# Kernel optimization log

Measured on AMD Instinct MI355X. Metric: run time of the kernel, lower is better.

## Reference

```python
import jax, jax.numpy as jnp
import numpy as np

DN = ('NCH', 'OIH', 'NCH')

def conv1d(x, w, b, stride, pad):
    y = jax.lax.conv_general_dilated(x, w, (stride,), [(pad, pad)], dimension_numbers=DN)
    return y + b[None, :, None]

def deconv1d(x, w, b):
    # ConvTranspose1d(k=3, stride=2, padding=1, output_padding=1): L -> 2L
    # expressed as lhs-dilated conv with padding (k-1-p, k-1-p+output_padding) = (1, 2)
    y = jax.lax.conv_general_dilated(x, w, (1,), [(1, 2)], lhs_dilation=(2,), dimension_numbers=DN)
    return y + b[None, :, None]

def setup_inputs() -> dict:
    key = jax.random.key(0)
    ks = jax.random.split(key, 24)
    B, T, A = 256, 512, 32
    H = 256              # hidden_dim / embedding_dim
    K = 8192             # n_embeddings
    enc_ch = [64, 128, 256]
    dec_ch = [256, 128, 64]
    s = 0.05
    inp = {'x': jax.random.normal(ks[0], (B, T, A), jnp.float32)}
    # encoder convs (OIH layout), k=3
    in_ch = A
    for i, ch in enumerate(enc_ch):
        inp[f'enc_w{i}'] = jax.random.normal(ks[1 + 2 * i], (ch, in_ch, 3), jnp.float32) * s
        inp[f'enc_b{i}'] = jnp.zeros((ch,), jnp.float32)
        in_ch = ch
    inp['proj_w'] = jax.random.normal(ks[8], (H, enc_ch[-1], 1), jnp.float32) * s
    inp['proj_b'] = jnp.zeros((H,), jnp.float32)
    inp['embedding'] = jax.random.normal(ks[9], (K, H), jnp.float32)
    # decoder deconvs (stored directly in conv OIH form)
    in_ch = H
    for i, ch in enumerate(dec_ch + [A]):
        inp[f'dec_w{i}'] = jax.random.normal(ks[10 + 2 * i], (ch, in_ch, 3), jnp.float32) * s
        inp[f'dec_b{i}'] = jnp.zeros((ch,), jnp.float32)
        in_ch = ch
    return inp

def _forward(x, enc_w0, enc_b0, enc_w1, enc_b1, enc_w2, enc_b2, proj_w, proj_b,
             embedding, dec_w0, dec_b0, dec_w1, dec_b1, dec_w2, dec_b2, dec_w3, dec_b3):
    # ---- encoder ----
    h = jnp.transpose(x, (0, 2, 1))                      # (B, A, T)
    h = jax.nn.relu(conv1d(h, enc_w0, enc_b0, 2, 1))
    h = jax.nn.relu(conv1d(h, enc_w1, enc_b1, 2, 1))
    h = jax.nn.relu(conv1d(h, enc_w2, enc_b2, 2, 1))
    z_e = conv1d(h, proj_w, proj_b, 1, 0)                # (B, H, T/8)
    # ---- EMA vector quantizer (eval-mode math) ----
    B, C, T = z_e.shape
    flat = jnp.transpose(z_e, (0, 2, 1)).reshape(-1, C)  # (B*T, C)
    dist = (jnp.sum(flat * flat, axis=1, keepdims=True)
            - 2.0 * flat @ embedding.T
            + jnp.sum(embedding * embedding, axis=1))    # (B*T, K)
    indices = jnp.argmin(dist, axis=1)                   # (B*T,)
    z_q = embedding[indices].reshape(B, T, C).transpose(0, 2, 1)  # (B, C, T)
    commitment_loss = jnp.mean((jax.lax.stop_gradient(z_e) - z_q) ** 2)
    codebook_loss = jnp.mean((z_e - jax.lax.stop_gradient(z_q)) ** 2)
    z_q = z_e + jax.lax.stop_gradient(z_q - z_e)         # straight-through
    # ---- decoder ----
    d = jax.nn.relu(deconv1d(z_q, dec_w0, dec_b0))
    d = jax.nn.relu(deconv1d(d, dec_w1, dec_b1))
    d = jax.nn.relu(deconv1d(d, dec_w2, dec_b2))
    d = deconv1d(d, dec_w3, dec_b3)                      # (B, A, seq_len)
    out = jnp.transpose(d, (0, 2, 1))                    # (B, seq_len, A)
    return out, codebook_loss, commitment_loss, indices.reshape(B, T)

def reference(x, enc_w0, enc_b0, enc_w1, enc_b1, enc_w2, enc_b2, proj_w, proj_b,
              embedding, dec_w0, dec_b0, dec_w1, dec_b1, dec_w2, dec_b2, dec_w3, dec_b3):
    return _forward(x, enc_w0, enc_b0, enc_w1, enc_b1, enc_w2, enc_b2, proj_w, proj_b,
                    embedding, dec_w0, dec_b0, dec_w1, dec_b1, dec_w2, dec_b2, dec_w3, dec_b3)
```

## Files before the change

kernel.cpp:

```cpp
#include <hip/hip_runtime.h>


typedef _Float16 half8 __attribute__((ext_vector_type(8)));
typedef _Float16 half4v __attribute__((ext_vector_type(4)));
typedef float f32x4 __attribute__((ext_vector_type(4)));
typedef float f32x16 __attribute__((ext_vector_type(16)));

struct CP2 {
  const _Float16* inH; const _Float16* inL;
  const _Float16* wH; const _Float16* wL;
  const float* bias;
  float* outF; _Float16* outH; _Float16* outL;
  const int* vidx;
  int Ci, lg2Ci, Ti, Co, To, K2, stride, pad, lg2U, Umask;
};

template<int SP, int PAR, bool GATHER, bool RELU, int OM>
__global__ __launch_bounds__(256, 4) void conv_mfma(CP2 p) {
  __shared__ _Float16 As[SP * 64 * 40];
  __shared__ _Float16 Bs[SP * 64 * 40];
  const int tid = threadIdx.x;
  const int wv = tid >> 6;
  const int lane = tid & 63;
  const int m = lane & 15, q = lane >> 4;
  const int btbase = blockIdx.x * 64;
  const int cobase = blockIdx.y * 64;
  f32x4 acc[4];
#pragma unroll
  for (int j = 0; j < 4; ++j) acc[j] = {0.f, 0.f, 0.f, 0.f};

  const int nkb = p.K2 >> 5;
  for (int kb = 0; kb < nkb; ++kb) {
    const int k0 = kb << 5;
    const int tap = k0 >> p.lg2Ci;
    const int ci0 = k0 & (p.Ci - 1);
    int dt;
    if (PAR == 0)      { dt = 0; }
    else if (PAR == 1) { dt = tap; }
    else               { dt = tap - p.pad; }
    __syncthreads();
    {
      const int wb = (blockIdx.y * nkb + kb) * 2048 + tid * 8;
      *(uint4*)&Bs[(tid >> 2) * 40 + (tid & 3) * 8] = *(const uint4*)&p.wH[wb];
      if (SP == 2)
        *(uint4*)&Bs[64 * 40 + (tid >> 2) * 40 + (tid & 3) * 8] = *(const uint4*)&p.wL[wb];
    }
    {
      const int r = tid >> 2, g = tid & 3;
      const int bt = btbase + r;
      const int b = bt >> p.lg2U, u = bt & p.Umask;
      const int tin = (PAR < 0) ? u * p.stride + dt : u + dt;
      const bool ok = (tin >= 0) && (tin < p.Ti);
      int ai;
      if (GATHER) {
        const int er = ok ? p.vidx[b * p.Ti + tin] : 0;
        ai = er * 256 + ci0 + g * 8;
      } else {
        ai = (b * p.Ti + tin) * p.Ci + ci0 + g * 8;
      }
      const uint4 z = {0u, 0u, 0u, 0u};
      const uint4 vh = ok ? *(const uint4*)&p.inH[ai] : z;
      *(uint4*)&As[r * 40 + g * 8] = vh;
      if (SP == 2) {
        const uint4 vl = ok ? *(const uint4*)&p.inL[ai] : z;
        *(uint4*)&As[64 * 40 + r * 40 + g * 8] = vl;
      }
    }
    __syncthreads();
    const int row = wv * 16 + m;
    const half8 a1 = *(const half8*)&As[row * 40 + q * 8];
    half8 a2;
    if (SP == 2) a2 = *(const half8*)&As[64 * 40 + row * 40 + q * 8];
#pragma unroll
    for (int ct = 0; ct < 4; ++ct) {
      const half8 b1 = *(const half8*)&Bs[(ct * 16 + m) * 40 + q * 8];
      half8 b2;
      if (SP == 2) b2 = *(const half8*)&Bs[64 * 40 + (ct * 16 + m) * 40 + q * 8];
      acc[ct] = __builtin_amdgcn_mfma_f32_16x16x32_f16(a1, b1, acc[ct], 0, 0, 0);
      if (SP == 2) {
        acc[ct] = __builtin_amdgcn_mfma_f32_16x16x32_f16(a2, b1, acc[ct], 0, 0, 0);
        acc[ct] = __builtin_amdgcn_mfma_f32_16x16x32_f16(a1, b2, acc[ct], 0, 0, 0);
      }
    }
  }
#pragma unroll
  for (int ct = 0; ct < 4; ++ct) {
    const int co = cobase + ct * 16 + m;
    if (co < p.Co) {
      const float bv = p.bias[co];
#pragma unroll
      for (int j = 0; j < 4; ++j) {
        const int row = btbase + wv * 16 + q * 4 + j;
        const int b = row >> p.lg2U, u = row & p.Umask;
        float v = acc[ct][j] + bv;
        if (RELU) v = fmaxf(v, 0.f);
        const int t = (PAR < 0) ? u : 2 * u + PAR;
        const int oi = (b * p.To + t) * p.Co + co;
        if (OM == 3) {
          p.outF[oi] = v;
        } else if (OM == 1) {
          p.outH[oi] = (_Float16)v;
        } else {
          const _Float16 h = (_Float16)v;
          const _Float16 l = (_Float16)(v - (float)h);
          p.outH[oi] = h; p.outL[oi] = l;
        }
      }
    }
  }
}

struct CPD {
  const _Float16* inH; const _Float16* wS; const float* bias;
  float* outF; _Float16* outH;
  int Ci, Ti, Co, To, lg2U, Umask;
};

template<bool RELU, bool F32OUT>
__global__ __launch_bounds__(256, 4) void conv_dec(CPD p) {
  __shared__ _Float16 As[65 * 40];
  __shared__ _Float16 Bs[3 * 64 * 40];
  const int tid = threadIdx.x;
  const int wv = tid >> 6;
  const int lane = tid & 63;
  const int m = lane & 15, q = lane >> 4;
  const int btbase = blockIdx.x * 64;
  const int cobase = blockIdx.y * 64;
  const int b0 = btbase >> p.lg2U;
  const int u0 = btbase & p.Umask;
  f32x4 aE[4], aO[4];
#pragma unroll
  for (int j = 0; j < 4; ++j) { aE[j] = {0.f,0.f,0.f,0.f}; aO[j] = {0.f,0.f,0.f,0.f}; }

  const int nkb = p.Ci >> 5;
  for (int kb = 0; kb < nkb; ++kb) {
    const int ci0 = kb << 5;
    __syncthreads();
    {
      const int wb = (blockIdx.y * nkb + kb) * 6144 + tid * 8;
      const int ld = (tid >> 2) * 40 + (tid & 3) * 8;
#pragma unroll
      for (int tap = 0; tap < 3; ++tap)
        *(uint4*)&Bs[tap * 2560 + ld] = *(const uint4*)&p.wS[wb + tap * 2048];
    }
#pragma unroll
    for (int i = 0; i < 2; ++i) {
      const int e = i * 256 + tid;
      const int r = e >> 2, g = e & 3;
      if (r < 65) {
        const int ur = u0 + r;
        const bool ok = ur < p.Ti;
        const uint4 z = {0u, 0u, 0u, 0u};
        const uint4 v = ok ? *(const uint4*)&p.inH[(b0 * p.Ti + ur) * p.Ci + ci0 + g * 8] : z;
        *(uint4*)&As[r * 40 + g * 8] = v;
      }
    }
    __syncthreads();
    const int row = wv * 16 + m;
    const half8 a0  = *(const half8*)&As[row * 40 + q * 8];
    const half8 a1s = *(const half8*)&As[(row + 1) * 40 + q * 8];
#pragma unroll
    for (int ct = 0; ct < 4; ++ct) {
      const int c = ct * 16 + m;
      const half8 w0 = *(const half8*)&Bs[c * 40 + q * 8];
      const half8 w1 = *(const half8*)&Bs[2560 + c * 40 + q * 8];
      const half8 w2 = *(const half8*)&Bs[5120 + c * 40 + q * 8];
      aE[ct] = __builtin_amdgcn_mfma_f32_16x16x32_f16(a0,  w1, aE[ct], 0, 0, 0);
      aO[ct] = __builtin_amdgcn_mfma_f32_16x16x32_f16(a0,  w0, aO[ct], 0, 0, 0);
      aO[ct] = __builtin_amdgcn_mfma_f32_16x16x32_f16(a1s, w2, aO[ct], 0, 0, 0);
    }
  }
#pragma unroll
  for (int ct = 0; ct < 4; ++ct) {
    const int co = cobase + ct * 16 + m;
    if (co < p.Co) {
      const float bv = p.bias[co];
#pragma unroll
      for (int j = 0; j < 4; ++j) {
        const int u = u0 + wv * 16 + q * 4 + j;
        float vE = aE[ct][j] + bv;
        float vO = aO[ct][j] + bv;
        if (RELU) { vE = fmaxf(vE, 0.f); vO = fmaxf(vO, 0.f); }
        const int oiE = (b0 * p.To + 2 * u) * p.Co + co;
        const int oiO = oiE + p.Co;
        if (F32OUT) { p.outF[oiE] = vE; p.outF[oiO] = vO; }
        else        { p.outH[oiE] = (_Float16)vE; p.outH[oiO] = (_Float16)vO; }
      }
    }
  }
}


__global__ __launch_bounds__(256) void x_prep(const float* __restrict__ x,
                                              _Float16* __restrict__ h,
                                              _Float16* __restrict__ l) {
  const int i = blockIdx.x * 256 + threadIdx.x;
  const float4 v = ((const float4*)x)[i];
  half4v a, b;
  a.x = (_Float16)v.x; b.x = (_Float16)(v.x - (float)a.x);
  a.y = (_Float16)v.y; b.y = (_Float16)(v.y - (float)a.y);
  a.z = (_Float16)v.z; b.z = (_Float16)(v.z - (float)a.z);
  a.w = (_Float16)v.w; b.w = (_Float16)(v.w - (float)a.w);
  ((half4v*)h)[i] = a;
  ((half4v*)l)[i] = b;
}

struct WPE { const float* w; int dh, dl, Ci, lg2Ci, KWO, Co, PAR, SP, nkb, base, dec; };
struct WPA { WPE e[9]; };

__global__ __launch_bounds__(256) void w_prep(WPA a, _Float16* __restrict__ wst) {
  const int b = (int)blockIdx.x;
  int i = 0;
#pragma unroll
  for (int j = 1; j < 9; ++j) if (b >= a.e[j].base) i = j;
  const WPE E = a.e[i];
  const int local = b - E.base;
  const int cb = local / E.nkb;
  const int kb = local - cb * E.nkb;
  const int tid = threadIdx.x;
  const int cc = tid >> 2, g = tid & 3;
  const int co = cb * 64 + cc;
  const bool okc = co < E.Co;
  const int k0 = kb << 5;
  const int tap0 = k0 >> E.lg2Ci;
  const int ci0 = k0 & (E.Ci - 1);
  if (!E.dec) {
    const int ko = (E.PAR == 0) ? 1 : (E.PAR == 1 ? 2 * tap0 : tap0);
    half8 hv, lv;
#pragma unroll
    for (int j = 0; j < 8; ++j) {
      const float wv = okc ? E.w[(co * E.Ci + ci0 + g * 8 + j) * E.KWO + ko] : 0.f;
      hv[j] = (_Float16)wv;
      lv[j] = (_Float16)(wv - (float)hv[j]);
    }
    const int off = (cb * E.nkb + kb) * 2048 + tid * 8;
    *(half8*)&wst[E.dh + off] = hv;
    if (E.SP == 2) *(half8*)&wst[E.dl + off] = lv;
  } else {
#pragma unroll
    for (int tap = 0; tap < 3; ++tap) {
      half8 hv;
#pragma unroll
      for (int j = 0; j < 8; ++j) {
        const float wv = okc ? E.w[(co * E.Ci + ci0 + g * 8 + j) * 3 + tap] : 0.f;
        hv[j] = (_Float16)wv;
      }
      *(half8*)&wst[E.dh + ((cb * E.nkb + kb) * 3 + tap) * 2048 + tid * 8] = hv;
    }
  }
}

__global__ __launch_bounds__(256) void emb_prep(const float* __restrict__ emb,
                                                _Float16* __restrict__ hi,
                                                _Float16* __restrict__ lo,
                                                float* __restrict__ nrm) {
  const int k = blockIdx.x * 4 + (threadIdx.x >> 6);
  const int lane = threadIdx.x & 63;
  const int i = k * 64 + lane;
  const float4 v = ((const float4*)emb)[i];
  half4v a, b;
  a.x = (_Float16)v.x; b.x = (_Float16)(v.x - (float)a.x);
  a.y = (_Float16)v.y; b.y = (_Float16)(v.y - (float)a.y);
  a.z = (_Float16)v.z; b.z = (_Float16)(v.z - (float)a.z);
  a.w = (_Float16)v.w; b.w = (_Float16)(v.w - (float)a.w);
  ((half4v*)hi)[i] = a;
  ((half4v*)lo)[i] = b;
  double s = (double)v.x * v.x + (double)v.y * v.y +
             (double)v.z * v.z + (double)v.w * v.w;
  for (int off = 32; off; off >>= 1) s += __shfl_down(s, off);
  if (lane == 0) nrm[k] = (float)s;
}

__global__ __launch_bounds__(256, 2) void vq_mfma(const _Float16* __restrict__ z1g,
                                                  const _Float16* __restrict__ z2g,
                                                  const _Float16* __restrict__ e1g,
                                                  const _Float16* __restrict__ e2g,
                                                  const float* __restrict__ nrm,
                                                  float* __restrict__ pbest,
                                                  int* __restrict__ pidx) {
  __shared__ _Float16 es[2 * 2 * 4096];
  const int tid = threadIdx.x;
  const int lane = tid & 63;
  const int w = tid >> 6;
  const int m32 = lane & 31;
  const int hi = lane >> 5;
  const int seg = blockIdx.x & 7, rb = blockIdx.x >> 3;
  const int rbase = rb * 128;
  const int row_g = rbase + w * 32 + m32;

  half8 za[16], zb[16];
#pragma unroll
  for (int c = 0; c < 16; ++c) {
    const int zi = row_g * 256 + c * 16 + hi * 8;
    za[c] = *(const half8*)&z1g[zi];
    zb[c] = *(const half8*)&z2g[zi];
  }

  float best[16]; int bk[16];
#pragma unroll
  for (int i = 0; i < 16; ++i) { best[i] = 3.4e38f; bk[i] = 0; }

  const int sbase = (seg * 1024 + ((tid >> 7) & 1) * 32 + (tid & 31)) * 256
                  + ((tid >> 6) & 1) * 16 + ((tid >> 5) & 1) * 8;
  const int lw = w * 512;

  auto stage = [&](int cc_, int kb_, int buf_) {
    const int off = sbase + cc_ * 32768 + kb_ * 32;
    __builtin_amdgcn_global_load_lds(
        (const __attribute__((address_space(1))) void*)(e1g + off),
        (__attribute__((address_space(3))) void*)&es[(buf_ * 2 + 0) * 4096 + lw], 16, 0, 0);
    __builtin_amdgcn_global_load_lds(
        (const __attribute__((address_space(1))) void*)(e1g + off + 16384),
        (__attribute__((address_space(3))) void*)&es[(buf_ * 2 + 0) * 4096 + 2048 + lw], 16, 0, 0);
    __builtin_amdgcn_global_load_lds(
        (const __attribute__((address_space(1))) void*)(e2g + off),
        (__attribute__((address_space(3))) void*)&es[(buf_ * 2 + 1) * 4096 + lw], 16, 0, 0);
    __builtin_amdgcn_global_load_lds(
        (const __attribute__((address_space(1))) void*)(e2g + off + 16384),
        (__attribute__((address_space(3))) void*)&es[(buf_ * 2 + 1) * 4096 + 2048 + lw], 16, 0, 0);
  };

  stage(0, 0, 0);

  const int lb = lane * 8;
  f32x16 acc[4];
  for (int cc = 0; cc < 8; ++cc) {
    const int cbase = seg * 1024 + cc * 128;
#pragma unroll
    for (int ct = 0; ct < 4; ++ct) {
#pragma unroll
      for (int rg = 0; rg < 16; ++rg) acc[ct][rg] = 0.f;
    }
#pragma unroll
    for (int kb = 0; kb < 8; ++kb) {
      const int buf = kb & 1;
      const _Float16* e1s = &es[(buf * 2 + 0) * 4096];
      const _Float16* e2s = &es[(buf * 2 + 1) * 4096];
      __syncthreads();
      if (kb < 7)      stage(cc, kb + 1, buf ^ 1);
      else if (cc < 7) stage(cc + 1, 0, buf ^ 1);
      __builtin_amdgcn_s_setprio(1);
#pragma unroll
      for (int ct = 0; ct < 4; ++ct) {
#pragma unroll
        for (int k16 = 0; k16 < 2; ++k16) {
          const half8 b1 = *(const half8*)&e1s[ct * 1024 + k16 * 512 + lb];
          const half8 b2 = *(const half8*)&e2s[ct * 1024 + k16 * 512 + lb];
          const half8 a1 = za[kb * 2 + k16];
          const half8 a2 = zb[kb * 2 + k16];
          acc[ct] = __builtin_amdgcn_mfma_f32_32x32x16_f16(a1, b1, acc[ct], 0, 0, 0);
          acc[ct] = __builtin_amdgcn_mfma_f32_32x32x16_f16(a2, b1, acc[ct], 0, 0, 0);
          acc[ct] = __builtin_amdgcn_mfma_f32_32x32x16_f16(a1, b2, acc[ct], 0, 0, 0);
        }
      }
      __builtin_amdgcn_s_setprio(0);
    }
#pragma unroll
    for (int ct = 0; ct < 4; ++ct) {
      const int k = cbase + ct * 32 + m32;
      const float nv = nrm[k];
#pragma unroll
      for (int rg = 0; rg < 16; ++rg) {
        const float d = nv - 2.f * acc[ct][rg];
        if (d < best[rg]) { best[rg] = d; bk[rg] = k; }
      }
    }
  }
#pragma unroll
  for (int rg = 0; rg < 16; ++rg) {
    float bv = best[rg]; int kv = bk[rg];
    for (int off = 1; off < 32; off <<= 1) {
      const float ob = __shfl_xor(bv, off);
      const int ok = __shfl_xor(kv, off);
      if (ob < bv || (ob == bv && ok < kv)) { bv = ob; kv = ok; }
    }
    if (m32 == 0) {
      const int row = rbase + w * 32 + (rg & 3) + 8 * (rg >> 2) + 4 * hi;
      pbest[seg * 16384 + row] = bv;
      pidx[seg * 16384 + row] = kv;
    }
  }
}

__global__ void merge_kernel(const float* __restrict__ pbest, const int* __restrict__ pidx,
                             int* __restrict__ vidx, float* __restrict__ out_idx,
                             float* __restrict__ lacc) {
  const int n = blockIdx.x * 256 + threadIdx.x;
  float bv = pbest[n]; int kv = pidx[n];
#pragma unroll
  for (int s = 1; s < 8; ++s) {
    const float ob = pbest[s * 16384 + n];
    const int ok = pidx[s * 16384 + n];
    if (ob < bv || (ob == bv && ok < kv)) { bv = ob; kv = ok; }
  }
  vidx[n] = kv;
  out_idx[n] = (float)kv;
  if (n == 0) *lacc = 0.f;
}

__global__ __launch_bounds__(256) void loss_kernel(const _Float16* __restrict__ z1g,
                                                   const _Float16* __restrict__ z2g,
                                                   const float* __restrict__ emb,
                                                   const int* __restrict__ vidx,
                                                   float* __restrict__ lacc) {
  const int g4 = blockIdx.x * 256 + threadIdx.x;
  const int e0 = g4 * 4;
  const int n = e0 >> 8, c = e0 & 255;
  const half4v a = ((const half4v*)z1g)[g4];
  const half4v b = ((const half4v*)z2g)[g4];
  const float4 q4 = *(const float4*)&emb[vidx[n] * 256 + c];
  const float dx = ((float)a.x + (float)b.x) - q4.x;
  const float dy = ((float)a.y + (float)b.y) - q4.y;
  const float dz = ((float)a.z + (float)b.z) - q4.z;
  const float dw = ((float)a.w + (float)b.w) - q4.w;
  float s = dx * dx + dy * dy + dz * dz + dw * dw;
  for (int off = 32; off; off >>= 1) s += __shfl_down(s, off);
  __shared__ float red[4];
  if ((threadIdx.x & 63) == 0) red[threadIdx.x >> 6] = s;
  __syncthreads();
  if (threadIdx.x == 0) atomicAdd(lacc, red[0] + red[1] + red[2] + red[3]);
}

__global__ void fin_kernel(const float* __restrict__ lacc, float* __restrict__ out, int loff) {
  if (threadIdx.x == 0) {
    const float l = *lacc * (1.f / 4194304.f);
    out[loff] = l;
    out[loff + 1] = l;
  }
}

extern "C" void kernel_launch(void* const* d_in, const int* in_sizes, int n_in,
                              void* d_out, int out_size, void* d_ws, size_t ws_size,
                              hipStream_t stream) {
  const float* x   = (const float*)d_in[0];
  const float* ew0 = (const float*)d_in[1];  const float* eb0 = (const float*)d_in[2];
  const float* ew1 = (const float*)d_in[3];  const float* eb1 = (const float*)d_in[4];
  const float* ew2 = (const float*)d_in[5];  const float* eb2 = (const float*)d_in[6];
  const float* pw  = (const float*)d_in[7];  const float* pb  = (const float*)d_in[8];
  const float* emb = (const float*)d_in[9];
  const float* dw0 = (const float*)d_in[10]; const float* db0 = (const float*)d_in[11];
  const float* dw1 = (const float*)d_in[12]; const float* db1 = (const float*)d_in[13];
  const float* dw2 = (const float*)d_in[14]; const float* db2 = (const float*)d_in[15];
  const float* dw3 = (const float*)d_in[16]; const float* db3 = (const float*)d_in[17];
  float* ws  = (float*)d_ws;
  float* out = (float*)d_out;

  const int A0 = 0, B0 = 4194304, C0 = 8388608, TL = 12582912;
  _Float16* h0h = (_Float16*)(ws + C0);
  _Float16* h0l = h0h + 4194304;
  _Float16* h1h = (_Float16*)(ws + B0);
  _Float16* h1l = h1h + 4194304;
  _Float16* h2h = (_Float16*)(ws + A0);
  _Float16* h2l = h2h + 4194304;
  _Float16* h3h = (_Float16*)(ws + B0);
  _Float16* h3l = h3h + 4194304;
  _Float16* z1g = (_Float16*)(ws + A0);
  _Float16* z2g = z1g + 4194304;
  _Float16* e1g = (_Float16*)(ws + B0);
  _Float16* e2g = e1g + 2097152;
  float* pbest = ws + B0 + 2097152;
  int*   pidx  = (int*)(ws + B0 + 2097152 + 131072);
  _Float16* d1h = (_Float16*)(ws + C0);
  _Float16* d2h = (_Float16*)(ws + A0);
  _Float16* d3h = (_Float16*)(ws + B0);
  float* nrm  = ws + TL;
  int*   vidx = (int*)(ws + TL + 8192);
  float* lacc = ws + TL + 8192 + 16384;
  _Float16* wst = (_Float16*)(ws + TL + 32768);

  const int W_E0H = 0,      W_E0L = 6144;
  const int W_E1H = 12288,  W_E1L = 36864;
  const int W_E2H = 61440,  W_E2L = 159744;
  const int W_PJH = 258048, W_PJL = 323584;
  const int W_D0A = 389120, W_D0B = 454656;
  const int W_DC1 = 585728, W_DC2 = 684032, W_DC3 = 708608;

  const int idx_off  = out_size - 16384;
  const int loss_off = out_size - 16386;

  x_prep<<<4096, 256, 0, stream>>>(x, h0h, h0l);
  WPA wa;
  wa.e[0] = {ew0, W_E0H, W_E0L, 32,  5, 3, 64,  -1, 2, 3,  0,   0};
  wa.e[1] = {ew1, W_E1H, W_E1L, 64,  6, 3, 128, -1, 2, 6,  3,   0};
  wa.e[2] = {ew2, W_E2H, W_E2L, 128, 7, 3, 256, -1, 2, 12, 15,  0};
  wa.e[3] = {pw,  W_PJH, W_PJL, 256, 8, 1, 256, -1, 2, 8,  63,  0};
  wa.e[4] = {dw0, W_D0A, 0,     256, 8, 3, 256,  0, 1, 8,  95,  0};
  wa.e[5] = {dw0, W_D0B, 0,     256, 8, 3, 256,  1, 1, 16, 127, 0};
  wa.e[6] = {dw1, W_DC1, 0,     256, 8, 3, 128, -1, 1, 8,  191, 1};
  wa.e[7] = {dw2, W_DC2, 0,     128, 7, 3, 64,  -1, 1, 4,  207, 1};
  wa.e[8] = {dw3, W_DC3, 0,     64,  6, 3, 32,  -1, 1, 2,  211, 1};
  w_prep<<<213, 256, 0, stream>>>(wa, wst);

  CP2 p; p.vidx = nullptr; p.inH = nullptr; p.inL = nullptr;
  p.outF = nullptr; p.outH = nullptr; p.outL = nullptr;

  p.inH = h0h; p.inL = h0l; p.wH = wst + W_E0H; p.wL = wst + W_E0L;
  p.bias = eb0; p.outH = h1h; p.outL = h1l;
  p.Ci = 32; p.lg2Ci = 5; p.Ti = 512; p.Co = 64; p.To = 256;
  p.K2 = 96; p.stride = 2; p.pad = 1; p.lg2U = 8; p.Umask = 255;
  conv_mfma<2, -1, false, true, 0><<<dim3(1024, 1), 256, 0, stream>>>(p);

  p.inH = h1h; p.inL = h1l; p.wH = wst + W_E1H; p.wL = wst + W_E1L;
  p.bias = eb1; p.outH = h2h; p.outL = h2l;
  p.Ci = 64; p.lg2Ci = 6; p.Ti = 256; p.Co = 128; p.To = 128; p.K2 = 192;
  p.lg2U = 7; p.Umask = 127;
  conv_mfma<2, -1, false, true, 0><<<dim3(512, 2), 256, 0, stream>>>(p);

  p.inH = h2h; p.inL = h2l; p.wH = wst + W_E2H; p.wL = wst + W_E2L;
  p.bias = eb2; p.outH = h3h; p.outL = h3l;
  p.Ci = 128; p.lg2Ci = 7; p.Ti = 128; p.Co = 256; p.To = 64; p.K2 = 384;
  p.lg2U = 6; p.Umask = 63;
  conv_mfma<2, -1, false, true, 0><<<dim3(256, 4), 256, 0, stream>>>(p);

  p.inH = h3h; p.inL = h3l; p.wH = wst + W_PJH; p.wL = wst + W_PJL;
  p.bias = pb; p.outH = z1g; p.outL = z2g;
  p.Ci = 256; p.lg2Ci = 8; p.Ti = 64; p.Co = 256; p.To = 64;
  p.K2 = 256; p.stride = 1; p.pad = 0; p.lg2U = 6; p.Umask = 63;
  conv_mfma<2, -1, false, false, 0><<<dim3(256, 4), 256, 0, stream>>>(p);

  emb_prep<<<2048, 256, 0, stream>>>(emb, e1g, e2g, nrm);
  vq_mfma<<<1024, 256, 0, stream>>>(z1g, z2g, e1g, e2g, nrm, pbest, pidx);
  merge_kernel<<<64, 256, 0, stream>>>(pbest, pidx, vidx, out + idx_off, lacc);
  loss_kernel<<<4096, 256, 0, stream>>>(z1g, z2g, emb, vidx, lacc);
  fin_kernel<<<1, 64, 0, stream>>>(lacc, out, loss_off);

  p.inH = e1g; p.inL = nullptr; p.bias = db0;
  p.outH = d1h; p.outL = nullptr; p.vidx = vidx;
  p.Ci = 256; p.lg2Ci = 8; p.Ti = 64; p.Co = 256; p.To = 128;
  p.lg2U = 6; p.Umask = 63;
  p.wH = wst + W_D0A; p.wL = nullptr;
  p.K2 = 256; conv_mfma<1, 0, true, true, 1><<<dim3(256, 4), 256, 0, stream>>>(p);
  p.wH = wst + W_D0B;
  p.K2 = 512; conv_mfma<1, 1, true, true, 1><<<dim3(256, 4), 256, 0, stream>>>(p);

  CPD d;
  d.inH = d1h; d.wS = wst + W_DC1; d.bias = db1; d.outF = nullptr; d.outH = d2h;
  d.Ci = 256; d.Ti = 128; d.Co = 128; d.To = 256; d.lg2U = 7; d.Umask = 127;
  conv_dec<true, false><<<dim3(512, 2), 256, 0, stream>>>(d);

  d.inH = d2h; d.wS = wst + W_DC2; d.bias = db2; d.outH = d3h;
  d.Ci = 128; d.Ti = 256; d.Co = 64; d.To = 512; d.lg2U = 8; d.Umask = 255;
  conv_dec<true, false><<<dim3(1024, 1), 256, 0, stream>>>(d);

  d.inH = d3h; d.wS = wst + W_DC3; d.bias = db3; d.outF = out; d.outH = nullptr;
  d.Ci = 64; d.Ti = 512; d.Co = 32; d.To = 1024; d.lg2U = 9; d.Umask = 511;
  conv_dec<false, true><<<dim3(2048, 1), 256, 0, stream>>>(d);
}
```

Baseline: 515.5 us.

## Double-buffer conv tiles using direct global-to-LDS loads

Both conv kernels now stage activation and weight tiles with direct global-to-LDS loads into two LDS buffers. The next K-block is prefetched while the current one feeds the MFMAs, leaving one barrier per iteration instead of two. Weights are pre-arranged into MFMA fragment order, and out-of-range rows read from a small zeroed pad buffer, so LDS reads become contiguous per lane. The aim is to hide global load latency and drop the register round-trip. The cost is twice the LDS per block, and correctness relies on the compiler inserting the right waits for the asynchronous LDS loads before each barrier.

```diff
diff --git a/kernel.cpp b/kernel.cpp
--- a/kernel.cpp
+++ b/kernel.cpp
@@ -6,10 +6,14 @@
 typedef float f32x4 __attribute__((ext_vector_type(4)));
 typedef float f32x16 __attribute__((ext_vector_type(16)));
 
+#define GL_LDS(src, dst) \
+  __builtin_amdgcn_global_load_lds((const __attribute__((address_space(1))) void*)(src), \
+                                   (__attribute__((address_space(3))) void*)(dst), 16, 0, 0)
+
 struct CP2 {
   const _Float16* inH; const _Float16* inL;
   const _Float16* wH; const _Float16* wL;
-  const float* bias;
+  const float* bias; const _Float16* zpad;
   float* outF; _Float16* outH; _Float16* outL;
   const int* vidx;
   int Ci, lg2Ci, Ti, Co, To, K2, stride, pad, lg2U, Umask;
@@ -17,65 +21,66 @@
 
 template<int SP, int PAR, bool GATHER, bool RELU, int OM>
 __global__ __launch_bounds__(256, 4) void conv_mfma(CP2 p) {
-  __shared__ _Float16 As[SP * 64 * 40];
-  __shared__ _Float16 Bs[SP * 64 * 40];
+  __shared__ _Float16 As[2][SP * 2048];
+  __shared__ _Float16 Bs[2][SP * 2048];
   const int tid = threadIdx.x;
-  const int wv = tid >> 6;
+  const int w = tid >> 6;
   const int lane = tid & 63;
   const int m = lane & 15, q = lane >> 4;
   const int btbase = blockIdx.x * 64;
   const int cobase = blockIdx.y * 64;
-  f32x4 acc[4];
-#pragma unroll
-  for (int j = 0; j < 4; ++j) acc[j] = {0.f, 0.f, 0.f, 0.f};
-
+  const int bt = btbase + w * 16 + m;
+  const int b = bt >> p.lg2U, u = bt & p.Umask;
   const int nkb = p.K2 >> 5;
-  for (int kb = 0; kb < nkb; ++kb) {
+  const int lw = w * 512;
+
+  int er0 = 0, er1 = 0;
+  if (GATHER) {
+    er0 = p.vidx[b * p.Ti + u];
+    if (PAR == 1) er1 = (u + 1 < p.Ti) ? p.vidx[b * p.Ti + u + 1] : 0;
+  }
+
+  auto stage = [&](int kb, int buf) {
     const int k0 = kb << 5;
     const int tap = k0 >> p.lg2Ci;
     const int ci0 = k0 & (p.Ci - 1);
     int dt;
-    if (PAR == 0)      { dt = 0; }
-    else if (PAR == 1) { dt = tap; }
-    else               { dt = tap - p.pad; }
+    if (PAR == 0)      dt = 0;
+    else if (PAR == 1) dt = tap;
+    else               dt = tap - p.pad;
+    const int tin = (PAR < 0) ? u * p.stride + dt : u + dt;
+    const bool ok = (tin >= 0) && (tin < p.Ti);
+    int ai;
+    if (GATHER) {
+      const int er = (PAR == 1 && tap == 1) ? er1 : er0;
+      ai = er * 256 + ci0 + q * 8;
+    } else {
+      ai = (b * p.Ti + tin) * p.Ci + ci0 + q * 8;
+    }
+    GL_LDS(ok ? &p.inH[ai] : p.zpad, &As[buf][lw]);
+    if (SP == 2) GL_LDS(ok ? &p.inL[ai] : p.zpad, &As[buf][2048 + lw]);
+    const int wb = (blockIdx.y * nkb + kb) * 2048 + lw + lane * 8;
+    GL_LDS(&p.wH[wb], &Bs[buf][lw]);
+    if (SP == 2) GL_LDS(&p.wL[wb], &Bs[buf][2048 + lw]);
+  };
+
+  f32x4 acc[4];
+#pragma unroll
+  for (int j = 0; j < 4; ++j) acc[j] = {0.f, 0.f, 0.f, 0.f};
+
+  stage(0, 0);
+  for (int kb = 0; kb < nkb; ++kb) {
+    const int buf = kb & 1;
     __syncthreads();
-    {
-      const int wb = (blockIdx.y * nkb + kb) * 2048 + tid * 8;
-      *(uint4*)&Bs[(tid >> 2) * 40 + (tid & 3) * 8] = *(const uint4*)&p.wH[wb];
-      if (SP == 2)
-        *(uint4*)&Bs[64 * 40 + (tid >> 2) * 40 + (tid & 3) * 8] = *(const uint4*)&p.wL[wb];
-    }
-    {
-      const int r = tid >> 2, g = tid & 3;
-      const int bt = btbase + r;
-      const int b = bt >> p.lg2U, u = bt & p.Umask;
-      const int tin = (PAR < 0) ? u * p.stride + dt : u + dt;
-      const bool ok = (tin >= 0) && (tin < p.Ti);
-      int ai;
-      if (GATHER) {
-        const int er = ok ? p.vidx[b * p.Ti + tin] : 0;
-        ai = er * 256 + ci0 + g * 8;
-      } else {
-        ai = (b * p.Ti + tin) * p.Ci + ci0 + g * 8;
-      }
-      const uint4 z = {0u, 0u, 0u, 0u};
-      const uint4 vh = ok ? *(const uint4*)&p.inH[ai] : z;
-      *(uint4*)&As[r * 40 + g * 8] = vh;
-      if (SP == 2) {
-        const uint4 vl = ok ? *(const uint4*)&p.inL[ai] : z;
-        *(uint4*)&As[64 * 40 + r * 40 + g * 8] = vl;
-      }
-    }
-    __syncthreads();
-    const int row = wv * 16 + m;
-    const half8 a1 = *(const half8*)&As[row * 40 + q * 8];
+    if (kb + 1 < nkb) stage(kb + 1, buf ^ 1);
+    const half8 a1 = *(const half8*)&As[buf][lw + lane * 8];
     half8 a2;
-    if (SP == 2) a2 = *(const half8*)&As[64 * 40 + row * 40 + q * 8];
+    if (SP == 2) a2 = *(const half8*)&As[buf][2048 + lw + lane * 8];
 #pragma unroll
     for (int ct = 0; ct < 4; ++ct) {
-      const half8 b1 = *(const half8*)&Bs[(ct * 16 + m) * 40 + q * 8];
+      const half8 b1 = *(const half8*)&Bs[buf][ct * 512 + lane * 8];
       half8 b2;
-      if (SP == 2) b2 = *(const half8*)&Bs[64 * 40 + (ct * 16 + m) * 40 + q * 8];
+      if (SP == 2) b2 = *(const half8*)&Bs[buf][2048 + ct * 512 + lane * 8];
       acc[ct] = __builtin_amdgcn_mfma_f32_16x16x32_f16(a1, b1, acc[ct], 0, 0, 0);
       if (SP == 2) {
         acc[ct] = __builtin_amdgcn_mfma_f32_16x16x32_f16(a2, b1, acc[ct], 0, 0, 0);
@@ -90,12 +95,12 @@
       const float bv = p.bias[co];
 #pragma unroll
       for (int j = 0; j < 4; ++j) {
-        const int row = btbase + wv * 16 + q * 4 + j;
-        const int b = row >> p.lg2U, u = row & p.Umask;
+        const int row = btbase + w * 16 + q * 4 + j;
+        const int bb = row >> p.lg2U, uu = row & p.Umask;
         float v = acc[ct][j] + bv;
         if (RELU) v = fmaxf(v, 0.f);
-        const int t = (PAR < 0) ? u : 2 * u + PAR;
-        const int oi = (b * p.To + t) * p.Co + co;
+        const int t = (PAR < 0) ? uu : 2 * uu + PAR;
+        const int oi = (bb * p.To + t) * p.Co + co;
         if (OM == 3) {
           p.outF[oi] = v;
         } else if (OM == 1) {
@@ -112,59 +117,65 @@
 
 struct CPD {
   const _Float16* inH; const _Float16* wS; const float* bias;
+  const _Float16* zpad;
   float* outF; _Float16* outH;
   int Ci, Ti, Co, To, lg2U, Umask;
 };
 
 template<bool RELU, bool F32OUT>
 __global__ __launch_bounds__(256, 4) void conv_dec(CPD p) {
-  __shared__ _Float16 As[65 * 40];
-  __shared__ _Float16 Bs[3 * 64 * 40];
+  __shared__ _Float16 As[2][2560];
+  __shared__ _Float16 Bs[2][6144];
   const int tid = threadIdx.x;
-  const int wv = tid >> 6;
+  const int w = tid >> 6;
   const int lane = tid & 63;
   const int m = lane & 15, q = lane >> 4;
   const int btbase = blockIdx.x * 64;
   const int cobase = blockIdx.y * 64;
   const int b0 = btbase >> p.lg2U;
   const int u0 = btbase & p.Umask;
+  const int nkb = p.Ci >> 5;
+  const int lw = w * 512;
+
+  auto stage = [&](int kb, int buf) {
+    const int ci0 = kb << 5;
+    {
+      const int ur = u0 + w * 16 + m;
+      const bool ok = ur < p.Ti;
+      GL_LDS(ok ? &p.inH[(b0 * p.Ti + ur) * p.Ci + ci0 + q * 8] : p.zpad,
+             &As[buf][lw]);
+    }
+    if (w == 0) {
+      const int ur = u0 + 64 + m;
+      const bool ok = ur < p.Ti;
+      GL_LDS(ok ? &p.inH[(b0 * p.Ti + ur) * p.Ci + ci0 + q * 8] : p.zpad,
+             &As[buf][2048]);
+    }
+    const int wb = (blockIdx.y * nkb + kb) * 6144;
+#pragma unroll
+    for (int tap = 0; tap < 3; ++tap)
+      GL_LDS(&p.wS[wb + tap * 2048 + lw + lane * 8], &Bs[buf][tap * 2048 + lw]);
+  };
+
   f32x4 aE[4], aO[4];
 #pragma unroll
   for (int j = 0; j < 4; ++j) { aE[j] = {0.f,0.f,0.f,0.f}; aO[j] = {0.f,0.f,0.f,0.f}; }
 
-  const int nkb = p.Ci >> 5;
+  stage(0, 0);
   for (int kb = 0; kb < nkb; ++kb) {
-    const int ci0 = kb << 5;
+    const int buf = kb & 1;
     __syncthreads();
-    {
-      const int wb = (blockIdx.y * nkb + kb) * 6144 + tid * 8;
-      const int ld = (tid >> 2) * 40 + (tid & 3) * 8;
-#pragma unroll
-      for (int tap = 0; tap < 3; ++tap)
-        *(uint4*)&Bs[tap * 2560 + ld] = *(const uint4*)&p.wS[wb + tap * 2048];
-    }
-#pragma unroll
-    for (int i = 0; i < 2; ++i) {
-      const int e = i * 256 + tid;
-      const int r = e >> 2, g = e & 3;
-      if (r < 65) {
-        const int ur = u0 + r;
-        const bool ok = ur < p.Ti;
-        const uint4 z = {0u, 0u, 0u, 0u};
-        const uint4 v = ok ? *(const uint4*)&p.inH[(b0 * p.Ti + ur) * p.Ci + ci0 + g * 8] : z;
-        *(uint4*)&As[r * 40 + g * 8] = v;
-      }
-    }
-    __syncthreads();
-    const int row = wv * 16 + m;
-    const half8 a0  = *(const half8*)&As[row * 40 + q * 8];
-    const half8 a1s = *(const half8*)&As[(row + 1) * 40 + q * 8];
+    if (kb + 1 < nkb) stage(kb + 1, buf ^ 1);
+    const int row = w * 16 + m;
+    const half8 a0 = *(const half8*)&As[buf][lw + lane * 8];
+    const int r1 = row + 1;
+    const int s1 = (r1 >> 4) * 512 + ((r1 & 15) + (q << 4)) * 8;
+    const half8 a1s = *(const half8*)&As[buf][s1];
 #pragma unroll
     for (int ct = 0; ct < 4; ++ct) {
-      const int c = ct * 16 + m;
-      const half8 w0 = *(const half8*)&Bs[c * 40 + q * 8];
-      const half8 w1 = *(const half8*)&Bs[2560 + c * 40 + q * 8];
-      const half8 w2 = *(const half8*)&Bs[5120 + c * 40 + q * 8];
+      const half8 w0 = *(const half8*)&Bs[buf][ct * 512 + lane * 8];
+      const half8 w1 = *(const half8*)&Bs[buf][2048 + ct * 512 + lane * 8];
+      const half8 w2 = *(const half8*)&Bs[buf][4096 + ct * 512 + lane * 8];
       aE[ct] = __builtin_amdgcn_mfma_f32_16x16x32_f16(a0,  w1, aE[ct], 0, 0, 0);
       aO[ct] = __builtin_amdgcn_mfma_f32_16x16x32_f16(a0,  w0, aO[ct], 0, 0, 0);
       aO[ct] = __builtin_amdgcn_mfma_f32_16x16x32_f16(a1s, w2, aO[ct], 0, 0, 0);
@@ -177,7 +188,7 @@
       const float bv = p.bias[co];
 #pragma unroll
       for (int j = 0; j < 4; ++j) {
-        const int u = u0 + wv * 16 + q * 4 + j;
+        const int u = u0 + w * 16 + q * 4 + j;
         float vE = aE[ct][j] + bv;
         float vO = aO[ct][j] + bv;
         if (RELU) { vE = fmaxf(vE, 0.f); vO = fmaxf(vO, 0.f); }
@@ -193,7 +204,12 @@
 
 __global__ __launch_bounds__(256) void x_prep(const float* __restrict__ x,
                                               _Float16* __restrict__ h,
-                                              _Float16* __restrict__ l) {
+                                              _Float16* __restrict__ l,
+                                              _Float16* __restrict__ zp) {
+  if (blockIdx.x == 0 && threadIdx.x < 64) {
+    const uint4 z = {0u, 0u, 0u, 0u};
+    ((uint4*)zp)[threadIdx.x] = z;
+  }
   const int i = blockIdx.x * 256 + threadIdx.x;
   const float4 v = ((const float4*)x)[i];
   half4v a, b;
@@ -224,6 +240,7 @@
   const int k0 = kb << 5;
   const int tap0 = k0 >> E.lg2Ci;
   const int ci0 = k0 & (E.Ci - 1);
+  const int slot = (cc >> 4) * 512 + ((cc & 15) + (g << 4)) * 8;
   if (!E.dec) {
     const int ko = (E.PAR == 0) ? 1 : (E.PAR == 1 ? 2 * tap0 : tap0);
     half8 hv, lv;
@@ -233,7 +250,7 @@
       hv[j] = (_Float16)wv;
       lv[j] = (_Float16)(wv - (float)hv[j]);
     }
-    const int off = (cb * E.nkb + kb) * 2048 + tid * 8;
+    const int off = (cb * E.nkb + kb) * 2048 + slot;
     *(half8*)&wst[E.dh + off] = hv;
     if (E.SP == 2) *(half8*)&wst[E.dl + off] = lv;
   } else {
@@ -245,7 +262,7 @@
         const float wv = okc ? E.w[(co * E.Ci + ci0 + g * 8 + j) * 3 + tap] : 0.f;
         hv[j] = (_Float16)wv;
       }
-      *(half8*)&wst[E.dh + ((cb * E.nkb + kb) * 3 + tap) * 2048 + tid * 8] = hv;
+      *(half8*)&wst[E.dh + ((cb * E.nkb + kb) * 3 + tap) * 2048 + slot] = hv;
     }
   }
 }
@@ -466,6 +483,7 @@
   float* nrm  = ws + TL;
   int*   vidx = (int*)(ws + TL + 8192);
   float* lacc = ws + TL + 8192 + 16384;
+  _Float16* zpad = (_Float16*)(ws + TL + 26624);
   _Float16* wst = (_Float16*)(ws + TL + 32768);
 
   const int W_E0H = 0,      W_E0L = 6144;
@@ -478,7 +496,7 @@
   const int idx_off  = out_size - 16384;
   const int loss_off = out_size - 16386;
 
-  x_prep<<<4096, 256, 0, stream>>>(x, h0h, h0l);
+  x_prep<<<4096, 256, 0, stream>>>(x, h0h, h0l, zpad);
   WPA wa;
   wa.e[0] = {ew0, W_E0H, W_E0L, 32,  5, 3, 64,  -1, 2, 3,  0,   0};
   wa.e[1] = {ew1, W_E1H, W_E1L, 64,  6, 3, 128, -1, 2, 6,  3,   0};
@@ -492,7 +510,7 @@
   w_prep<<<213, 256, 0, stream>>>(wa, wst);
 
   CP2 p; p.vidx = nullptr; p.inH = nullptr; p.inL = nullptr;
-  p.outF = nullptr; p.outH = nullptr; p.outL = nullptr;
+  p.outF = nullptr; p.outH = nullptr; p.outL = nullptr; p.zpad = zpad;
 
   p.inH = h0h; p.inL = h0l; p.wH = wst + W_E0H; p.wL = wst + W_E0L;
   p.bias = eb0; p.outH = h1h; p.outL = h1l;
@@ -533,7 +551,7 @@
   p.wH = wst + W_D0B;
   p.K2 = 512; conv_mfma<1, 1, true, true, 1><<<dim3(256, 4), 256, 0, stream>>>(p);
 
-  CPD d;
+  CPD d; d.zpad = zpad;
   d.inH = d1h; d.wS = wst + W_DC1; d.bias = db1; d.outF = nullptr; d.outH = d2h;
   d.Ci = 256; d.Ti = 128; d.Co = 128; d.To = 256; d.lg2U = 7; d.Umask = 127;
   conv_dec<true, false><<<dim3(512, 2), 256, 0, stream>>>(d);
```

Result: faster. 498.4 us, median of 3 (-3.3%).
